# Kernel tuning notes

Measured on AMD Instinct MI355X. Metric: run time of the kernel, lower is better.

Reference implementation:

```python
import jax, jax.numpy as jnp
import numpy as np
from jax import lax

EPS = 1e-8  # torch F.cosine_similarity per-norm clamp


def setup_inputs() -> dict:
    key = jax.random.key(0)
    k1, k2, k3 = jax.random.split(key, 3)
    bs, c_in, nodes, length = 64, 64, 307, 12
    c_out = c_in // 4  # 16
    x = jax.random.normal(k1, (bs, c_in, nodes, length), dtype=jnp.float32)
    # Conv2d weight [O, I, 1, 3], kaiming-ish scale
    w = jax.random.normal(k2, (c_out, c_in, 1, 3), dtype=jnp.float32) / np.sqrt(c_in * 3)
    b = jax.random.normal(k3, (c_out,), dtype=jnp.float32) * 0.01
    return {"x": x, "w": w, "b": b}


def reference(x, w, b):
    # Conv2d kernel (1,3), padding (0,1): [bs, C', N, L]
    y = lax.conv_general_dilated(
        x, w, window_strides=(1, 1), padding=((0, 0), (1, 1)),
        dimension_numbers=("NCHW", "OIHW", "NCHW"))
    y = y + b[None, :, None, None]

    # nodeb = last timestep features: [bs, C', N]
    last = y[..., -1]

    # Fused cosine similarity: dot over channel dim, normalized per-vector
    dot = jnp.einsum("bci,bcjt->bijt", last, y)          # [bs, N, N, L]
    n_last = jnp.linalg.norm(last, axis=1)                 # [bs, N]
    n_all = jnp.linalg.norm(y, axis=1)                     # [bs, N, L]
    denom = (jnp.maximum(n_last, EPS)[:, :, None, None] *
             jnp.maximum(n_all, EPS)[:, None, :, :])
    return dot / denom  # [bs, N, N, L]
```

## Files before the change

### kernel.cpp

```cpp
#include <hip/hip_runtime.h>

typedef float v4f __attribute__((ext_vector_type(4)));

#define B_   64
#define CIN  64
#define CO   16
#define NN   307
#define LL   12
#define JT   (NN * LL)
#define LHP  320

__global__ void repack_w_kernel(const float* __restrict__ w, float* __restrict__ wt) {
    int t = blockIdx.x * 256 + threadIdx.x;
    if (t < CO * CIN * 3) {
        int o = t & 15;
        int k = (t >> 4) % 3;
        int i = t / 48;
        wt[i * 48 + k * 16 + o] = w[(o * CIN + i) * 3 + k];
    }
}

__global__ __launch_bounds__(256) void conv_norm_kernel(
    const float* __restrict__ x, const float* __restrict__ wt,
    const float* __restrict__ bias, float* __restrict__ yhat,
    float* __restrict__ lhat) {
    int tid = blockIdx.x * 256 + threadIdx.x;
    int b   = tid / JT;
    int rem = tid - b * JT;
    int n   = rem / LL;
    int l   = rem - n * LL;

    const float* xp = x + (size_t)b * CIN * JT + rem;

    float acc[CO];
#pragma unroll
    for (int o = 0; o < CO; ++o) acc[o] = bias[o];

    const int   offm = (l > 0) ? -1 : 0;
    const int   offp = (l < LL - 1) ? 1 : 0;
    const float mm   = (l > 0) ? 1.f : 0.f;
    const float mp   = (l < LL - 1) ? 1.f : 0.f;

#pragma unroll 4
    for (int i = 0; i < CIN; ++i) {
        const float* xr = xp + i * JT;
        float xm = xr[offm] * mm;
        float x0 = xr[0];
        float xq = xr[offp] * mp;
        const float* wr = wt + i * 48;
#pragma unroll
        for (int o = 0; o < CO; ++o) {
            acc[o] += wr[o] * xm + wr[16 + o] * x0 + wr[32 + o] * xq;
        }
    }

    float ss = 0.f;
#pragma unroll
    for (int o = 0; o < CO; ++o) ss += acc[o] * acc[o];
    float inv = 1.f / fmaxf(sqrtf(ss), 1e-8f);

    float* yp = yhat + (size_t)b * CO * JT + rem;
#pragma unroll
    for (int o = 0; o < CO; ++o) yp[o * JT] = acc[o] * inv;

    if (l == LL - 1) {
        float* lp = lhat + (size_t)b * CO * LHP + n;
#pragma unroll
        for (int o = 0; o < CO; ++o) lp[o * LHP] = acc[o] * inv;
    }
}

__global__ __launch_bounds__(256) void cos_kernel(
    const float* __restrict__ yhat, const float* __restrict__ lhat,
    float* __restrict__ out) {
    const int b    = blockIdx.z;
    const int i0   = blockIdx.x * 16;
    const int jt0  = blockIdx.y * 512;
    const int lane = threadIdx.x & 63;
    const int wv   = threadIdx.x >> 6;
    const int ib   = i0 + wv * 4;
    const int jtA  = jt0 + lane * 4;
    const int jtB  = jtA + 256;
    const bool vA  = (jtA < JT);
    const bool vB  = (jtB < JT);

    const float* lp = lhat + (size_t)b * CO * LHP + ib;
    v4f lt[CO];
#pragma unroll
    for (int c = 0; c < CO; ++c) lt[c] = *(const v4f*)(lp + c * LHP);

    const float* yb = yhat + (size_t)b * CO * JT;

    v4f accA[4], accB[4];
#pragma unroll
    for (int r = 0; r < 4; ++r) { accA[r] = (v4f)0.f; accB[r] = (v4f)0.f; }

#pragma unroll
    for (int c = 0; c < CO; ++c) {
        v4f ya = vA ? *(const v4f*)(yb + c * JT + jtA) : (v4f)0.f;
        v4f yz = vB ? *(const v4f*)(yb + c * JT + jtB) : (v4f)0.f;
#pragma unroll
        for (int r = 0; r < 4; ++r) {
            float lv = lt[c][r];
            accA[r] += lv * ya;
            accB[r] += lv * yz;
        }
    }

#pragma unroll
    for (int r = 0; r < 4; ++r) {
        int i = ib + r;
        if (i < NN) {
            float* op = out + ((size_t)b * NN + i) * JT;
            if (vA) *(v4f*)(op + jtA) = accA[r];
            if (vB) *(v4f*)(op + jtB) = accB[r];
        }
    }
}

extern "C" void kernel_launch(void* const* d_in, const int* in_sizes, int n_in,
                              void* d_out, int out_size, void* d_ws, size_t ws_size,
                              hipStream_t stream) {
    const float* x    = (const float*)d_in[0];
    const float* w    = (const float*)d_in[1];
    const float* bias = (const float*)d_in[2];
    float* out = (float*)d_out;

    float* ws   = (float*)d_ws;
    float* yhat = ws;
    float* lhat = yhat + (size_t)B_ * CO * JT;
    float* wt   = lhat + (size_t)B_ * CO * LHP;

    repack_w_kernel<<<(CO * CIN * 3 + 255) / 256, 256, 0, stream>>>(w, wt);

    conv_norm_kernel<<<(B_ * JT) / 256, 256, 0, stream>>>(x, wt, bias, yhat, lhat);

    dim3 g(20, 8, B_);
    cos_kernel<<<g, 256, 0, stream>>>(yhat, lhat, out);
}
```

Baseline: 408.5 us.

## Fuse conv-normalize into cosine kernel via shared-memory strip tiles

Replaces the separate conv/normalize kernel and the yhat workspace with a strip kernel. Each block computes the normalized conv output for a 256-column chunk into LDS, then loops over all 307 rows of last-timestep vectors to write the output strip. A small dedicated kernel computes only the last-timestep normalized features, using two taps. This removes the global round trip of the intermediate tensor, but cuts the grid to 960 blocks with a long serial loop per block, which may lower the parallelism available for hiding store latency.

```diff
diff --git a/kernel.cpp b/kernel.cpp
--- a/kernel.cpp
+++ b/kernel.cpp
@@ -2,13 +2,16 @@
 
 typedef float v4f __attribute__((ext_vector_type(4)));
 
-#define B_   64
-#define CIN  64
-#define CO   16
-#define NN   307
-#define LL   12
-#define JT   (NN * LL)
-#define LHP  320
+#define B_     64
+#define CIN    64
+#define CO     16
+#define NN     307
+#define LL     12
+#define JT     (NN * LL)
+#define LHP    320
+#define CHUNK  256
+#define NCHUNK 15
+#define NRG    20
 
 __global__ void repack_w_kernel(const float* __restrict__ w, float* __restrict__ wt) {
     int t = blockIdx.x * 256 + threadIdx.x;
@@ -20,17 +23,54 @@
     }
 }
 
-__global__ __launch_bounds__(256) void conv_norm_kernel(
+__global__ __launch_bounds__(256) void lhat_kernel(
     const float* __restrict__ x, const float* __restrict__ wt,
-    const float* __restrict__ bias, float* __restrict__ yhat,
-    float* __restrict__ lhat) {
+    const float* __restrict__ bias, float* __restrict__ lhat) {
     int tid = blockIdx.x * 256 + threadIdx.x;
-    int b   = tid / JT;
-    int rem = tid - b * JT;
-    int n   = rem / LL;
-    int l   = rem - n * LL;
+    if (tid >= B_ * NN) return;
+    int b = tid / NN, n = tid - b * NN;
+    const float* xp = x + (size_t)b * CIN * JT + n * LL + (LL - 1);
 
-    const float* xp = x + (size_t)b * CIN * JT + rem;
+    float acc[CO];
+#pragma unroll
+    for (int o = 0; o < CO; ++o) acc[o] = bias[o];
+
+#pragma unroll 4
+    for (int i = 0; i < CIN; ++i) {
+        float xm = xp[i * JT - 1];
+        float x0 = xp[i * JT];
+        const float* wr = wt + i * 48;
+#pragma unroll
+        for (int o = 0; o < CO; ++o)
+            acc[o] += wr[o] * xm + wr[16 + o] * x0;
+    }
+
+    float ss = 0.f;
+#pragma unroll
+    for (int o = 0; o < CO; ++o) ss += acc[o] * acc[o];
+    float inv = 1.f / fmaxf(sqrtf(ss), 1e-8f);
+
+    float* lp = lhat + (size_t)b * CO * LHP + n;
+#pragma unroll
+    for (int o = 0; o < CO; ++o) lp[o * LHP] = acc[o] * inv;
+}
+
+__global__ __launch_bounds__(256) void strip_kernel(
+    const float* __restrict__ x, const float* __restrict__ wt,
+    const float* __restrict__ bias, const float* __restrict__ lhat,
+    float* __restrict__ out) {
+    __shared__ float ylds[CO][CHUNK];
+
+    const int b   = blockIdx.y;
+    const int jt0 = blockIdx.x * CHUNK;
+    const int t   = threadIdx.x;
+
+    int jt  = jt0 + t;
+    int jtc = (jt < JT) ? jt : (JT - 1);
+    int n   = jtc / LL;
+    int l   = jtc - n * LL;
+
+    const float* xp = x + (size_t)b * CIN * JT + jtc;
 
     float acc[CO];
 #pragma unroll
@@ -49,9 +89,8 @@
         float xq = xr[offp] * mp;
         const float* wr = wt + i * 48;
 #pragma unroll
-        for (int o = 0; o < CO; ++o) {
+        for (int o = 0; o < CO; ++o)
             acc[o] += wr[o] * xm + wr[16 + o] * x0 + wr[32 + o] * xq;
-        }
     }
 
     float ss = 0.f;
@@ -59,61 +98,42 @@
     for (int o = 0; o < CO; ++o) ss += acc[o] * acc[o];
     float inv = 1.f / fmaxf(sqrtf(ss), 1e-8f);
 
-    float* yp = yhat + (size_t)b * CO * JT + rem;
 #pragma unroll
-    for (int o = 0; o < CO; ++o) yp[o * JT] = acc[o] * inv;
+    for (int o = 0; o < CO; ++o) ylds[o][t] = acc[o] * inv;
 
-    if (l == LL - 1) {
-        float* lp = lhat + (size_t)b * CO * LHP + n;
+    __syncthreads();
+
+    const int lane = t & 63;
+    const int wv   = t >> 6;
+    const int jtA  = jt0 + lane * 4;
+    const bool vA  = (jtA < JT);
+
+    v4f y[CO];
 #pragma unroll
-        for (int o = 0; o < CO; ++o) lp[o * LHP] = acc[o] * inv;
-    }
-}
+    for (int c = 0; c < CO; ++c) y[c] = *(const v4f*)&ylds[c][lane * 4];
 
-__global__ __launch_bounds__(256) void cos_kernel(
-    const float* __restrict__ yhat, const float* __restrict__ lhat,
-    float* __restrict__ out) {
-    const int b    = blockIdx.z;
-    const int i0   = blockIdx.x * 16;
-    const int jt0  = blockIdx.y * 512;
-    const int lane = threadIdx.x & 63;
-    const int wv   = threadIdx.x >> 6;
-    const int ib   = i0 + wv * 4;
-    const int jtA  = jt0 + lane * 4;
-    const int jtB  = jtA + 256;
-    const bool vA  = (jtA < JT);
-    const bool vB  = (jtB < JT);
+    const float* lb = lhat + (size_t)b * CO * LHP;
+    float* ob = out + (size_t)b * NN * JT + jtA;
 
-    const float* lp = lhat + (size_t)b * CO * LHP + ib;
-    v4f lt[CO];
+    for (int rg = 0; rg < NRG; ++rg) {
+        const int ib = rg * 16 + wv * 4;
+        const float* lp = lb + ib;
+
+        v4f a0 = (v4f)0.f, a1 = (v4f)0.f, a2 = (v4f)0.f, a3 = (v4f)0.f;
 #pragma unroll
-    for (int c = 0; c < CO; ++c) lt[c] = *(const v4f*)(lp + c * LHP);
+        for (int c = 0; c < CO; ++c) {
+            v4f lt = *(const v4f*)(lp + c * LHP);
+            a0 += lt[0] * y[c];
+            a1 += lt[1] * y[c];
+            a2 += lt[2] * y[c];
+            a3 += lt[3] * y[c];
+        }
 
-    const float* yb = yhat + (size_t)b * CO * JT;
-
-    v4f accA[4], accB[4];
-#pragma unroll
-    for (int r = 0; r < 4; ++r) { accA[r] = (v4f)0.f; accB[r] = (v4f)0.f; }
-
-#pragma unroll
-    for (int c = 0; c < CO; ++c) {
-        v4f ya = vA ? *(const v4f*)(yb + c * JT + jtA) : (v4f)0.f;
-        v4f yz = vB ? *(const v4f*)(yb + c * JT + jtB) : (v4f)0.f;
-#pragma unroll
-        for (int r = 0; r < 4; ++r) {
-            float lv = lt[c][r];
-            accA[r] += lv * ya;
-            accB[r] += lv * yz;
-        }
-    }
-
-#pragma unroll
-    for (int r = 0; r < 4; ++r) {
-        int i = ib + r;
-        if (i < NN) {
-            float* op = out + ((size_t)b * NN + i) * JT;
-            if (vA) *(v4f*)(op + jtA) = accA[r];
-            if (vB) *(v4f*)(op + jtB) = accB[r];
+        if (vA) {
+            if (ib + 0 < NN) *(v4f*)(ob + (size_t)(ib + 0) * JT) = a0;
+            if (ib + 1 < NN) *(v4f*)(ob + (size_t)(ib + 1) * JT) = a1;
+            if (ib + 2 < NN) *(v4f*)(ob + (size_t)(ib + 2) * JT) = a2;
+            if (ib + 3 < NN) *(v4f*)(ob + (size_t)(ib + 3) * JT) = a3;
         }
     }
 }
@@ -127,14 +147,13 @@
     float* out = (float*)d_out;
 
     float* ws   = (float*)d_ws;
-    float* yhat = ws;
-    float* lhat = yhat + (size_t)B_ * CO * JT;
+    float* lhat = ws;
     float* wt   = lhat + (size_t)B_ * CO * LHP;
 
     repack_w_kernel<<<(CO * CIN * 3 + 255) / 256, 256, 0, stream>>>(w, wt);
 
-    conv_norm_kernel<<<(B_ * JT) / 256, 256, 0, stream>>>(x, wt, bias, yhat, lhat);
+    lhat_kernel<<<(B_ * NN + 255) / 256, 256, 0, stream>>>(x, wt, bias, lhat);
 
-    dim3 g(20, 8, B_);
-    cos_kernel<<<g, 256, 0, stream>>>(yhat, lhat, out);
+    dim3 g(NCHUNK, B_);
+    strip_kernel<<<g, 256, 0, stream>>>(x, wt, bias, lhat, out);
 }
```

Result: slower. 430.3 us (+5.3%).

## Remap workgroups across XCDs and enlarge cosine row tile with LDS staging

Applied to the files above, without the earlier changes.

Workgroup IDs in both the conv and cosine kernels are remapped so that consecutive logical tiles are placed on the same XCD, with the conv grid padded to a multiple of eight. The cosine kernel now handles 32 rows per block instead of 16, staging the normalized last-timestep vectors in shared memory. Each thread therefore reuses every yhat load across 8 output rows, which cuts yhat reads, and the XCD-aware ordering is meant to improve L2 locality. The cost is more accumulator registers and an added __syncthreads. Since the kernel is dominated by writing its large output, the gain may be small.

```diff
diff --git a/kernel.cpp b/kernel.cpp
--- a/kernel.cpp
+++ b/kernel.cpp
@@ -9,6 +9,15 @@
 #define LL   12
 #define JT   (NN * LL)
 #define LHP  320
+
+#define NRB  10
+#define NCB  8
+#define NWG  (NRB * NCB * B_)
+#define WPX  (NWG / 8)
+
+#define NCONV   ((B_ * JT) / 256)
+#define NCONV_P 928
+#define CPX     (NCONV_P / 8)
 
 __global__ void repack_w_kernel(const float* __restrict__ w, float* __restrict__ wt) {
     int t = blockIdx.x * 256 + threadIdx.x;
@@ -24,7 +33,9 @@
     const float* __restrict__ x, const float* __restrict__ wt,
     const float* __restrict__ bias, float* __restrict__ yhat,
     float* __restrict__ lhat) {
-    int tid = blockIdx.x * 256 + threadIdx.x;
+    int wg = (blockIdx.x & 7) * CPX + (blockIdx.x >> 3);
+    if (wg >= NCONV) return;
+    int tid = wg * 256 + threadIdx.x;
     int b   = tid / JT;
     int rem = tid - b * JT;
     int n   = rem / LL;
@@ -73,47 +84,65 @@
 __global__ __launch_bounds__(256) void cos_kernel(
     const float* __restrict__ yhat, const float* __restrict__ lhat,
     float* __restrict__ out) {
-    const int b    = blockIdx.z;
-    const int i0   = blockIdx.x * 16;
-    const int jt0  = blockIdx.y * 512;
-    const int lane = threadIdx.x & 63;
-    const int wv   = threadIdx.x >> 6;
-    const int ib   = i0 + wv * 4;
-    const int jtA  = jt0 + lane * 4;
-    const int jtB  = jtA + 256;
-    const bool vA  = (jtA < JT);
-    const bool vB  = (jtB < JT);
+    __shared__ float lsh[CO][32];
 
-    const float* lp = lhat + (size_t)b * CO * LHP + ib;
-    v4f lt[CO];
+    const int wgid = (blockIdx.x & 7) * WPX + (blockIdx.x >> 3);
+    const int rb   = wgid % NRB;
+    const int rem  = wgid / NRB;
+    const int cb   = rem & 7;
+    const int b    = rem >> 3;
+
+    const int i0  = rb * 32;
+    const int jt0 = cb * 512;
+    const int t   = threadIdx.x;
+
+    {
+        const float* lb = lhat + (size_t)b * CO * LHP + i0;
 #pragma unroll
-    for (int c = 0; c < CO; ++c) lt[c] = *(const v4f*)(lp + c * LHP);
+        for (int k = 0; k < 2; ++k) {
+            int idx = t + k * 256;
+            int c = idx >> 5, j = idx & 31;
+            lsh[c][j] = lb[c * LHP + j];
+        }
+    }
+    __syncthreads();
 
-    const float* yb = yhat + (size_t)b * CO * JT;
+    const int lane = t & 63;
+    const int wv   = t >> 6;
+    const int wrow = wv * 8;
+    const int jl   = jt0 + lane * 4;
+    const bool vA  = (jl < JT);
+    const bool vB  = (jl + 256 < JT);
 
-    v4f accA[4], accB[4];
+    const float* yb = yhat + (size_t)b * CO * JT + jl;
+
+    v4f accA[8], accB[8];
 #pragma unroll
-    for (int r = 0; r < 4; ++r) { accA[r] = (v4f)0.f; accB[r] = (v4f)0.f; }
+    for (int r = 0; r < 8; ++r) { accA[r] = (v4f)0.f; accB[r] = (v4f)0.f; }
 
 #pragma unroll
     for (int c = 0; c < CO; ++c) {
-        v4f ya = vA ? *(const v4f*)(yb + c * JT + jtA) : (v4f)0.f;
-        v4f yz = vB ? *(const v4f*)(yb + c * JT + jtB) : (v4f)0.f;
+        const float* yc = yb + c * JT;
+        v4f yA = vA ? *(const v4f*)(yc + 0)   : (v4f)0.f;
+        v4f yB = vB ? *(const v4f*)(yc + 256) : (v4f)0.f;
+        v4f l0 = *(const v4f*)&lsh[c][wrow];
+        v4f l1 = *(const v4f*)&lsh[c][wrow + 4];
 #pragma unroll
         for (int r = 0; r < 4; ++r) {
-            float lv = lt[c][r];
-            accA[r] += lv * ya;
-            accB[r] += lv * yz;
+            accA[r]     += l0[r] * yA;
+            accB[r]     += l0[r] * yB;
+            accA[4 + r] += l1[r] * yA;
+            accB[4 + r] += l1[r] * yB;
         }
     }
 
 #pragma unroll
-    for (int r = 0; r < 4; ++r) {
-        int i = ib + r;
+    for (int r = 0; r < 8; ++r) {
+        int i = i0 + wrow + r;
         if (i < NN) {
-            float* op = out + ((size_t)b * NN + i) * JT;
-            if (vA) *(v4f*)(op + jtA) = accA[r];
-            if (vB) *(v4f*)(op + jtB) = accB[r];
+            float* op = out + ((size_t)b * NN + i) * JT + jl;
+            if (vA) *(v4f*)(op + 0)   = accA[r];
+            if (vB) *(v4f*)(op + 256) = accB[r];
         }
     }
 }
@@ -133,8 +162,7 @@
 
     repack_w_kernel<<<(CO * CIN * 3 + 255) / 256, 256, 0, stream>>>(w, wt);
 
-    conv_norm_kernel<<<(B_ * JT) / 256, 256, 0, stream>>>(x, wt, bias, yhat, lhat);
+    conv_norm_kernel<<<NCONV_P, 256, 0, stream>>>(x, wt, bias, yhat, lhat);
 
-    dim3 g(20, 8, B_);
-    cos_kernel<<<g, 256, 0, stream>>>(yhat, lhat, out);
+    cos_kernel<<<NWG, 256, 0, stream>>>(yhat, lhat, out);
 }
```

Result: no change. 405.1 us (-0.8%).
